# Kernel tuning notes

Hardware: AMD Instinct MI355X
Metric: run time of the kernel (lower is better)

Reference implementation:

```python
import jax, jax.numpy as jnp
import numpy as np

N_NODES = 20000
N_EDGES = 640000
HIDDEN = 256
HEADS = 8
HEAD_DIM = HIDDEN // HEADS
VOCAB = 119
N_FEATS = 9


def setup_inputs() -> dict:
    key = jax.random.key(0)
    ks = jax.random.split(key, 12)
    X = jax.random.randint(ks[0], (N_NODES, N_FEATS), 0, VOCAB)
    edge_row = jnp.sort(jax.random.randint(ks[1], (N_EDGES,), 0, N_NODES))
    edge_col = jax.random.randint(ks[2], (N_EDGES,), 0, N_NODES)
    s = 0.05  # init scale to keep activations sane
    emb_tables = jax.random.normal(ks[3], (N_FEATS, VOCAB, HIDDEN), jnp.float32) * s
    q_w = jax.random.normal(ks[4], (HIDDEN, HIDDEN), jnp.float32) * s
    q_b = jax.random.normal(ks[5], (HIDDEN,), jnp.float32) * s
    k_w = jax.random.normal(ks[6], (HIDDEN, HIDDEN), jnp.float32) * s
    k_b = jax.random.normal(ks[7], (HIDDEN,), jnp.float32) * s
    v_w = jax.random.normal(ks[8], (HIDDEN, HIDDEN), jnp.float32) * s
    v_b = jax.random.normal(ks[9], (HIDDEN,), jnp.float32) * s
    o_w = jax.random.normal(ks[10], (HIDDEN, HIDDEN), jnp.float32) * s
    o_b = jax.random.normal(ks[11], (HIDDEN,), jnp.float32) * s
    return dict(X=X, edge_row=edge_row, edge_col=edge_col, emb_tables=emb_tables,
                q_w=q_w, q_b=q_b, k_w=k_w, k_b=k_b, v_w=v_w, v_b=v_b, o_w=o_w, o_b=o_b)


def reference(X, edge_row, edge_col, emb_tables, q_w, q_b, k_w, k_b, v_w, v_b, o_w, o_b):
    N = X.shape[0]
    # AtomEncoder: sum of per-feature embeddings -> [N, HIDDEN]
    feat_idx = jnp.arange(N_FEATS)[None, :]  # [1, 9]
    h = emb_tables[feat_idx, X].sum(axis=1)  # [N, 9, H] -> [N, H]
    # q/k/v projections (torch Linear: y = x W^T + b), split into heads
    q = (h @ q_w.T + q_b).reshape(N, HEADS, HEAD_DIM) * (HEAD_DIM ** -0.5)
    k = (h @ k_w.T + k_b).reshape(N, HEADS, HEAD_DIM)
    v = (h @ v_w.T + v_b).reshape(N, HEADS, HEAD_DIM)
    # SDDMM: per-edge, per-head scores
    s = jnp.einsum('ehd,ehd->eh', q[edge_row], k[edge_col])  # [E, HEADS]
    # sparse row-wise softmax (over each node's outgoing-edge neighbors)
    m = jax.ops.segment_max(s, edge_row, num_segments=N)
    e = jnp.exp(s - m[edge_row])
    z = jax.ops.segment_sum(e, edge_row, num_segments=N)
    attn = e / z[edge_row]  # [E, HEADS]
    # SPMM: weighted aggregation of neighbor values
    out = jax.ops.segment_sum(attn[:, :, None] * v[edge_col], edge_row, num_segments=N)
    return out.reshape(N, HIDDEN) @ o_w.T + o_b
```

## Files before the change

kernel.cpp:

```cpp
#include <hip/hip_runtime.h>
#include <hip/hip_bf16.h>

#define N_NODES 20000
#define N_EDGES 640000
#define HIDDEN 256
#define HEADS 8
#define HEAD_DIM 32
#define N_FEATS 9
#define VOCAB 119

typedef __hip_bfloat16 bf16;
typedef __attribute__((ext_vector_type(8))) short short8;
typedef __attribute__((ext_vector_type(4))) float f32x4;
typedef __attribute__((ext_vector_type(2))) float f32x2;

__device__ __forceinline__ ushort f2u(float x) { union { ushort u; bf16 b; } c; c.b = __float2bfloat16(x); return c.u; }

__device__ __forceinline__ f32x2 pk_fma(f32x2 a, f32x2 b, f32x2 c) {
    f32x2 d;
    asm("v_pk_fma_f32 %0, %1, %2, %3" : "=v"(d) : "v"(a), "v"(b), "v"(c));
    return d;
}
__device__ __forceinline__ f32x2 pk_add(f32x2 a, f32x2 b) {
    f32x2 d;
    asm("v_pk_add_f32 %0, %1, %2" : "=v"(d) : "v"(a), "v"(b));
    return d;
}

template <int CTRL>
__device__ __forceinline__ float dpp_xor(float v) {
    return __int_as_float(__builtin_amdgcn_update_dpp(
        0, __float_as_int(v), CTRL, 0xf, 0xf, true));
}

__device__ __forceinline__ float fast_exp2(float x) {
#if __has_builtin(__builtin_amdgcn_exp2f)
    return __builtin_amdgcn_exp2f(x);
#else
    return exp2f(x);
#endif
}

__device__ __forceinline__ void sched_fence() {
    __builtin_amdgcn_sched_barrier(0);
}

#if __has_builtin(__builtin_amdgcn_fdot2_f32_bf16)
typedef __attribute__((ext_vector_type(2))) __bf16 bf16x2_t;
__device__ __forceinline__ float dot2bf(uint a, uint b, float c) {
    return __builtin_amdgcn_fdot2_f32_bf16(__builtin_bit_cast(bf16x2_t, a),
                                           __builtin_bit_cast(bf16x2_t, b), c, false);
}
#else
__device__ __forceinline__ float dot2bf(uint a, uint b, float c) {
    return c + __uint_as_float(a << 16) * __uint_as_float(b << 16)
             + __uint_as_float(a & 0xffff0000u) * __uint_as_float(b & 0xffff0000u);
}
#endif

__global__ void k_pre(const int* __restrict__ X, const float* __restrict__ emb,
                      bf16* __restrict__ h,
                      const float* __restrict__ qw, const float* __restrict__ kw,
                      const float* __restrict__ vw, const float* __restrict__ ow,
                      const float* __restrict__ qb, const float* __restrict__ kb,
                      const float* __restrict__ vb,
                      bf16* __restrict__ wqkv, bf16* __restrict__ wo,
                      float* __restrict__ qkvb,
                      const int* __restrict__ erow, int* __restrict__ row_ptr) {
    int b = blockIdx.x;
    if (b < 5000) {
        int tid = b * 256 + threadIdx.x;
        int n = tid >> 6;
        int c4 = (tid & 63) * 4;
        float4 a = make_float4(0.f, 0.f, 0.f, 0.f);
#pragma unroll
        for (int f = 0; f < N_FEATS; ++f) {
            int idx = X[n * N_FEATS + f];
            float4 e = *(const float4*)(emb + ((size_t)(f * VOCAB + idx)) * HIDDEN + c4);
            a.x += e.x; a.y += e.y; a.z += e.z; a.w += e.w;
        }
        ushort4 o = make_ushort4(f2u(a.x), f2u(a.y), f2u(a.z), f2u(a.w));
        *(ushort4*)((ushort*)h + (size_t)n * HIDDEN + c4) = o;
    } else if (b < 6027) {
        int i = (b - 5000) * 256 + threadIdx.x;
        if (i < 196608) {
            const float* s = i < 65536 ? qw : i < 131072 ? kw : vw;
            wqkv[i] = __float2bfloat16(s[i & 65535]);
        } else if (i < 262144) {
            wo[i - 196608] = __float2bfloat16(ow[i - 196608]);
        } else if (i < 262912) {
            int j = i - 262144;
            const float* s = j < 256 ? qb : j < 512 ? kb : vb;
            qkvb[j] = s[j & 255];
        }
    } else {
        int n = (b - 6027) * 256 + threadIdx.x;
        if (n > N_NODES) return;
        int lo = 0, hi = N_EDGES;
        while (lo < hi) {
            int mid = (lo + hi) >> 1;
            if (erow[mid] < n) lo = mid + 1; else hi = mid;
        }
        row_ptr[n] = lo;
    }
}

template <int MODE, bool GUARD, int TM>
__device__ __forceinline__ void gemm_core(const bf16* __restrict__ A,
                                          const bf16* __restrict__ W,
                                          const float* __restrict__ bias,
                                          void* __restrict__ Y0, void* __restrict__ Y1,
                                          float s_q, int n0, int d0) {
    constexpr int RI = TM / 32;
    __shared__ short As[TM * 72];
    __shared__ short Bs[128 * 72];
    int t = threadIdx.x;
    int lane = t & 63, w = t >> 6;
    int wr = (w >> 1) * (TM / 2), wc = (w & 1) * 64;
    int lr = lane & 15, quad = lane >> 4;

    f32x4 acc[RI][4] = {};
    short8 ra[RI], rb[4];
    int srowA[RI], skoA[RI], srowB[4], skoB[4];
#pragma unroll
    for (int it = 0; it < RI; ++it) { int c = t + 256 * it; srowA[it] = c >> 3; skoA[it] = (c & 7) * 8; }
#pragma unroll
    for (int it = 0; it < 4; ++it) { int c = t + 256 * it; srowB[it] = c >> 3; skoB[it] = (c & 7) * 8; }

#pragma unroll
    for (int it = 0; it < RI; ++it) {
        int n = n0 + srowA[it];
        short8 av = {};
        if (!GUARD || n < N_NODES) av = *(const short8*)(A + (size_t)n * HIDDEN + skoA[it]);
        ra[it] = av;
    }
#pragma unroll
    for (int it = 0; it < 4; ++it)
        rb[it] = *(const short8*)(W + (size_t)(d0 + srowB[it]) * HIDDEN + skoB[it]);
#pragma unroll
    for (int it = 0; it < RI; ++it) *(short8*)(&As[srowA[it] * 72 + skoA[it]]) = ra[it];
#pragma unroll
    for (int it = 0; it < 4; ++it)  *(short8*)(&Bs[srowB[it] * 72 + skoB[it]]) = rb[it];
    __syncthreads();

    for (int k0 = 64; k0 < 256; k0 += 64) {
#pragma unroll
        for (int it = 0; it < RI; ++it) {
            int n = n0 + srowA[it];
            short8 av = {};
            if (!GUARD || n < N_NODES) av = *(const short8*)(A + (size_t)n * HIDDEN + k0 + skoA[it]);
            ra[it] = av;
        }
#pragma unroll
        for (int it = 0; it < 4; ++it)
            rb[it] = *(const short8*)(W + (size_t)(d0 + srowB[it]) * HIDDEN + k0 + skoB[it]);
        {
            short8 af[RI][2], bfr[4][2];
#pragma unroll
            for (int i = 0; i < RI; ++i)
#pragma unroll
                for (int kk = 0; kk < 2; ++kk)
                    af[i][kk] = *(short8*)(&As[(wr + i * 16 + lr) * 72 + kk * 32 + quad * 8]);
#pragma unroll
            for (int j = 0; j < 4; ++j)
#pragma unroll
                for (int kk = 0; kk < 2; ++kk)
                    bfr[j][kk] = *(short8*)(&Bs[(wc + j * 16 + lr) * 72 + kk * 32 + quad * 8]);
#pragma unroll
            for (int kk = 0; kk < 2; ++kk)
#pragma unroll
                for (int i = 0; i < RI; ++i)
#pragma unroll
                    for (int j = 0; j < 4; ++j)
                        acc[i][j] = __builtin_amdgcn_mfma_f32_16x16x32_bf16(
                            af[i][kk], bfr[j][kk], acc[i][j], 0, 0, 0);
        }
        __syncthreads();
#pragma unroll
        for (int it = 0; it < RI; ++it) *(short8*)(&As[srowA[it] * 72 + skoA[it]]) = ra[it];
#pragma unroll
        for (int it = 0; it < 4; ++it)  *(short8*)(&Bs[srowB[it] * 72 + skoB[it]]) = rb[it];
        __syncthreads();
    }
    {
        short8 af[RI][2], bfr[4][2];
#pragma unroll
        for (int i = 0; i < RI; ++i)
#pragma unroll
            for (int kk = 0; kk < 2; ++kk)
                af[i][kk] = *(short8*)(&As[(wr + i * 16 + lr) * 72 + kk * 32 + quad * 8]);
#pragma unroll
        for (int j = 0; j < 4; ++j)
#pragma unroll
            for (int kk = 0; kk < 2; ++kk)
                bfr[j][kk] = *(short8*)(&Bs[(wc + j * 16 + lr) * 72 + kk * 32 + quad * 8]);
#pragma unroll
        for (int kk = 0; kk < 2; ++kk)
#pragma unroll
            for (int i = 0; i < RI; ++i)
#pragma unroll
                for (int j = 0; j < 4; ++j)
                    acc[i][j] = __builtin_amdgcn_mfma_f32_16x16x32_bf16(
                        af[i][kk], bfr[j][kk], acc[i][j], 0, 0, 0);
    }

#pragma unroll
    for (int j = 0; j < 4; ++j) {
        int dbase = d0 + wc + j * 16;
        float bj = bias[dbase + lr];
        if constexpr (MODE == 0) {
            float sc = (dbase < 256) ? s_q : 1.f;
            ushort* dst; int stride;
            if (dbase < 256) {
                dst = (ushort*)Y0 + (size_t)(dbase >> 6) * N_NODES * 64 + (dbase & 63) + lr;
                stride = 64;
            } else if (dbase < 512) {
                int e = dbase - 256;
                dst = (ushort*)Y1 + (size_t)(e >> 6) * N_NODES * 128 + (e & 63) + lr;
                stride = 128;
            } else {
                int e = dbase - 512;
                dst = (ushort*)Y1 + (size_t)(e >> 6) * N_NODES * 128 + 64 + (e & 63) + lr;
                stride = 128;
            }
#pragma unroll
            for (int i = 0; i < RI; ++i)
#pragma unroll
                for (int r = 0; r < 4; ++r) {
                    int n = n0 + wr + i * 16 + quad * 4 + r;
                    if (GUARD && n >= N_NODES) continue;
                    dst[(size_t)n * stride] = f2u((acc[i][j][r] + bj) * sc);
                }
        } else {
            float* dst = (float*)Y0 + dbase + lr;
#pragma unroll
            for (int i = 0; i < RI; ++i)
#pragma unroll
                for (int r = 0; r < 4; ++r) {
                    int n = n0 + wr + i * 16 + quad * 4 + r;
                    if (GUARD && n >= N_NODES) continue;
                    dst[(size_t)n * HIDDEN] = acc[i][j][r] + bj;
                }
        }
    }
}

__global__ __launch_bounds__(256, 2) void k_gemm_qkv(
    const bf16* __restrict__ A, const bf16* __restrict__ wqkv,
    const float* __restrict__ qkvb, ushort* __restrict__ qhp,
    ushort* __restrict__ kvhp, float qscale) {
    int n0 = blockIdx.x * 128;
    if (n0 + 128 <= N_NODES)
        gemm_core<0, false, 128>(A, wqkv, qkvb, qhp, kvhp, qscale, n0, blockIdx.y * 128);
    else
        gemm_core<0, true, 128>(A, wqkv, qkvb, qhp, kvhp, qscale, n0, blockIdx.y * 128);
}

__global__ __launch_bounds__(256, 4) void k_gemm_o(
    const bf16* __restrict__ A, const bf16* __restrict__ W,
    const float* __restrict__ bias, float* __restrict__ Y) {
    int n0 = blockIdx.x * 64;
    if (n0 + 64 <= N_NODES)
        gemm_core<1, false, 64>(A, W, bias, Y, nullptr, 1.f, n0, blockIdx.y * 128);
    else
        gemm_core<1, true, 64>(A, W, bias, Y, nullptr, 1.f, n0, blockIdx.y * 128);
}


template <int NIT>
__device__ __forceinline__ void pv_accum(const uint4* vv, const float* pb,
                                         f32x2& av0, f32x2& av1, f32x2& av2v, f32x2& av3) {
#pragma unroll
    for (int it = 0; it < NIT; ++it) {
        f32x2 pp; pp.x = pb[it]; pp.y = pb[it];
        f32x2 vf0, vf1, vf2, vf3;
        vf0.x = __uint_as_float(vv[it].x << 16); vf0.y = __uint_as_float(vv[it].x & 0xffff0000u);
        vf1.x = __uint_as_float(vv[it].y << 16); vf1.y = __uint_as_float(vv[it].y & 0xffff0000u);
        vf2.x = __uint_as_float(vv[it].z << 16); vf2.y = __uint_as_float(vv[it].z & 0xffff0000u);
        vf3.x = __uint_as_float(vv[it].w << 16); vf3.y = __uint_as_float(vv[it].w & 0xffff0000u);
        av0  = pk_fma(vf0, pp, av0);
        av1  = pk_fma(vf1, pp, av1);
        av2v = pk_fma(vf2, pp, av2v);
        av3  = pk_fma(vf3, pp, av3);
    }
}

__device__ __forceinline__ void attn_combine(int lane, int d8, float z,
                                             f32x2 av0, f32x2 av1, f32x2 av2v, f32x2 av3,
                                             ushort* __restrict__ orow) {
    bool b3 = (lane & 8) != 0, b4 = (lane & 16) != 0, b5 = (lane & 32) != 0;
    f32x2 sd0 = b3 ? av0 : av2v;
    f32x2 sd1 = b3 ? av1 : av3;
    f32x2 r0, r1;
    r0.x = dpp_xor<0x128>(sd0.x); r0.y = dpp_xor<0x128>(sd0.y);
    r1.x = dpp_xor<0x128>(sd1.x); r1.y = dpp_xor<0x128>(sd1.y);
    f32x2 t0 = pk_add(b3 ? av2v : av0, r0);
    f32x2 t1 = pk_add(b3 ? av3  : av1, r1);
    f32x2 sdu = b4 ? t0 : t1;
    f32x2 ru; ru.x = __shfl_xor(sdu.x, 16); ru.y = __shfl_xor(sdu.y, 16);
    f32x2 u = pk_add(b4 ? t1 : t0, ru);
    float sw = b5 ? u.x : u.y;
    float rw = __shfl_xor(sw, 32);
    float w = (b5 ? u.y : u.x) + rw;
    int dim = d8 * 8 + ((lane >> 3) & 1) * 4 + ((lane >> 4) & 1) * 2 + ((lane >> 5) & 1);
    orow[dim] = f2u(w * (1.f / z));
}

template <int NIT>
__device__ __forceinline__ void attn_dense(const int* __restrict__ cb, int deg,
                                           int lane, int my, int d8,
                                           const ushort* __restrict__ qrow,
                                           const ushort* __restrict__ kvbase,
                                           ushort* __restrict__ orow) {
    int degm8 = deg - my;
    uint d8b = (uint)d8 * 8;

    int cc[NIT];
#pragma unroll
    for (int it = 0; it < NIT; ++it) cc[it] = cb[min(it * 8 + my, deg - 1)];

    uint4 qu = *(const uint4*)(qrow + d8b);
    uint4 kk[NIT], vv[NIT];
#pragma unroll
    for (int it = 0; it < NIT; ++it)
        kk[it] = *(const uint4*)(kvbase + (((size_t)(uint)cc[it]) << 7) + d8b);
#pragma unroll
    for (int it = 0; it < NIT; ++it)
        vv[it] = *(const uint4*)(kvbase + (((size_t)(uint)cc[it]) << 7) + 64 + d8b);

    sched_fence();

    float z = 0.f;
    float pb[NIT];
#pragma unroll
    for (int it = 0; it < NIT; ++it) {
        float s = dot2bf(kk[it].x, qu.x, 0.f);
        s = dot2bf(kk[it].y, qu.y, s);
        s = dot2bf(kk[it].z, qu.z, s);
        s = dot2bf(kk[it].w, qu.w, s);
        s += dpp_xor<0xB1>(s);
        s += dpp_xor<0x4E>(s);
        float p = (it * 8 < degm8) ? fast_exp2(s) : 0.f;
        z += p;
        pb[it] = p;
    }
    z += dpp_xor<0x128>(z);
    z += __shfl_xor(z, 16);
    z += __shfl_xor(z, 32);

    f32x2 av0 = {0.f, 0.f}, av1 = {0.f, 0.f}, av2v = {0.f, 0.f}, av3 = {0.f, 0.f};
    pv_accum<NIT>(vv, pb, av0, av1, av2v, av3);
    attn_combine(lane, d8, z, av0, av1, av2v, av3, orow);
}

__global__ __launch_bounds__(256, 4) void k_attn(
    const int* __restrict__ row_ptr, const int* __restrict__ col,
    const ushort* __restrict__ qhp, const ushort* __restrict__ kvhp,
    bf16* __restrict__ agg) {
    int b = blockIdx.x;
    int x = b & 7;
    int hp = x & 3;
    int wave = __builtin_amdgcn_readfirstlane((int)(threadIdx.x >> 6));
    int n = (b >> 3) * 8 + (x >> 2) * 4 + wave;
    int lane = threadIdx.x & 63;
    int my = lane >> 3;
    int d8 = lane & 7;

    int start = row_ptr[n];
    int deg = row_ptr[n + 1] - start;

    ushort* orow = (ushort*)agg + (size_t)n * HIDDEN + hp * 64;
    if (deg == 0) {
        if (lane < 8) { uint4 zo = {}; *(uint4*)(orow + lane * 8) = zo; }
        return;
    }

    const ushort* qrow = qhp + ((size_t)hp * N_NODES + n) * 64;
    const ushort* kvbase = kvhp + (size_t)hp * N_NODES * 128;
    const int* cb = col + start;

    if (deg <= 32) {
        attn_dense<4>(cb, deg, lane, my, d8, qrow, kvbase, orow);
    } else if (deg <= 64) {
        attn_dense<8>(cb, deg, lane, my, d8, qrow, kvbase, orow);
    } else {
        uint4 qu = *(const uint4*)(qrow + d8 * 8);
        float z = 0.f;
        f32x2 av0 = {0.f, 0.f}, av1 = {0.f, 0.f}, av2v = {0.f, 0.f}, av3 = {0.f, 0.f};
        for (int i = 0; i < deg; i += 8) {
            int idx = i + my;
            int cidx = idx < deg ? idx : deg - 1;
            int c = cb[cidx];
            const ushort* kp = kvbase + (((size_t)(uint)c) << 7) + (uint)d8 * 8;
            uint4 ku = *(const uint4*)(kp);
            uint4 vu = *(const uint4*)(kp + 64);
            float s = dot2bf(ku.x, qu.x, 0.f);
            s = dot2bf(ku.y, qu.y, s);
            s = dot2bf(ku.z, qu.z, s);
            s = dot2bf(ku.w, qu.w, s);
            s += dpp_xor<0xB1>(s);
            s += dpp_xor<0x4E>(s);
            float p = (idx < deg) ? fast_exp2(s) : 0.f;
            z += p;
            f32x2 pp; pp.x = p; pp.y = p;
            f32x2 vf0, vf1, vf2, vf3;
            vf0.x = __uint_as_float(vu.x << 16); vf0.y = __uint_as_float(vu.x & 0xffff0000u);
            vf1.x = __uint_as_float(vu.y << 16); vf1.y = __uint_as_float(vu.y & 0xffff0000u);
            vf2.x = __uint_as_float(vu.z << 16); vf2.y = __uint_as_float(vu.z & 0xffff0000u);
            vf3.x = __uint_as_float(vu.w << 16); vf3.y = __uint_as_float(vu.w & 0xffff0000u);
            av0  = pk_fma(vf0, pp, av0);
            av1  = pk_fma(vf1, pp, av1);
            av2v = pk_fma(vf2, pp, av2v);
            av3  = pk_fma(vf3, pp, av3);
        }
        z += dpp_xor<0x128>(z);
        z += __shfl_xor(z, 16);
        z += __shfl_xor(z, 32);
        attn_combine(lane, d8, z, av0, av1, av2v, av3, orow);
    }
}

extern "C" void kernel_launch(void* const* d_in, const int* in_sizes, int n_in,
                              void* d_out, int out_size, void* d_ws, size_t ws_size,
                              hipStream_t stream) {
    const int*   X    = (const int*)d_in[0];
    const int*   erow = (const int*)d_in[1];
    const int*   ecol = (const int*)d_in[2];
    const float* emb  = (const float*)d_in[3];
    const float* q_w  = (const float*)d_in[4];
    const float* q_b  = (const float*)d_in[5];
    const float* k_w  = (const float*)d_in[6];
    const float* k_b  = (const float*)d_in[7];
    const float* v_w  = (const float*)d_in[8];
    const float* v_b  = (const float*)d_in[9];
    const float* o_w  = (const float*)d_in[10];
    const float* o_b  = (const float*)d_in[11];
    float* out = (float*)d_out;

    char* ws = (char*)d_ws;
    bf16*   h    = (bf16*)(ws);
    bf16*   agg  = (bf16*)(ws);
    ushort* qhp  = (ushort*)(ws + 10240000);
    ushort* kvhp = (ushort*)(ws + 20480000);
    bf16*   wqkv = (bf16*)(ws + 40960000);
    bf16*   wo   = (bf16*)(ws + 41353216);
    float*  qkvb = (float*)(ws + 41484288);
    int* row_ptr = (int*)(ws + 41487360);

    k_pre<<<6106, 256, 0, stream>>>(X, emb, h, q_w, k_w, v_w, o_w,
                                    q_b, k_b, v_b, wqkv, wo, qkvb, erow, row_ptr);

    const float qscale = 0.25503486121587466f;
    dim3 gqkv((N_NODES + 127) / 128, 768 / 128);
    k_gemm_qkv<<<gqkv, 256, 0, stream>>>(h, wqkv, qkvb, qhp, kvhp, qscale);

    k_attn<<<N_NODES, 256, 0, stream>>>(row_ptr, ecol, qhp, kvhp, agg);

    dim3 go((N_NODES + 63) / 64, HIDDEN / 128);
    k_gemm_o<<<go, 256, 0, stream>>>(agg, wo, o_b, out);
}
```

Baseline: 174.7 us.

## Process two head-pairs per wave in attention and shrink QKV GEMM row tile

The attention kernel now has each wave handle two head-pairs for one node instead of one. This halves the grid and shares the column-index loads across both head-pairs. A new paired dense path issues all K/V gathers for both head-pairs up front and interleaves the score computation to expose more memory-level parallelism. Separately, the QKV GEMM row tile drops from 128 to 64 with higher occupancy bounds, giving more blocks. The cost is more registers per wave in the attention kernel and fewer waves overall.

```diff
diff --git a/kernel.cpp b/kernel.cpp
--- a/kernel.cpp
+++ b/kernel.cpp
@@ -245,15 +245,15 @@
     }
 }
 
-__global__ __launch_bounds__(256, 2) void k_gemm_qkv(
+__global__ __launch_bounds__(256, 4) void k_gemm_qkv(
     const bf16* __restrict__ A, const bf16* __restrict__ wqkv,
     const float* __restrict__ qkvb, ushort* __restrict__ qhp,
     ushort* __restrict__ kvhp, float qscale) {
-    int n0 = blockIdx.x * 128;
-    if (n0 + 128 <= N_NODES)
-        gemm_core<0, false, 128>(A, wqkv, qkvb, qhp, kvhp, qscale, n0, blockIdx.y * 128);
+    int n0 = blockIdx.x * 64;
+    if (n0 + 64 <= N_NODES)
+        gemm_core<0, false, 64>(A, wqkv, qkvb, qhp, kvhp, qscale, n0, blockIdx.y * 128);
     else
-        gemm_core<0, true, 128>(A, wqkv, qkvb, qhp, kvhp, qscale, n0, blockIdx.y * 128);
+        gemm_core<0, true, 64>(A, wqkv, qkvb, qhp, kvhp, qscale, n0, blockIdx.y * 128);
 }
 
 __global__ __launch_bounds__(256, 4) void k_gemm_o(
@@ -353,70 +353,153 @@
     attn_combine(lane, d8, z, av0, av1, av2v, av3, orow);
 }
 
+__device__ __forceinline__ void attn_dense_pair(const int* __restrict__ cb, int deg,
+                                                int lane, int my, int d8,
+                                                const ushort* __restrict__ qrow0,
+                                                const ushort* __restrict__ qrow1,
+                                                const ushort* __restrict__ kvb0,
+                                                const ushort* __restrict__ kvb1,
+                                                ushort* __restrict__ orow0,
+                                                ushort* __restrict__ orow1) {
+    int degm8 = deg - my;
+    uint d8b = (uint)d8 * 8;
+
+    int cc[4];
+#pragma unroll
+    for (int it = 0; it < 4; ++it) cc[it] = cb[min(it * 8 + my, deg - 1)];
+
+    uint4 qu0 = *(const uint4*)(qrow0 + d8b);
+    uint4 qu1 = *(const uint4*)(qrow1 + d8b);
+    uint4 kk0[4], kk1[4], vv0[4], vv1[4];
+#pragma unroll
+    for (int it = 0; it < 4; ++it)
+        kk0[it] = *(const uint4*)(kvb0 + (((size_t)(uint)cc[it]) << 7) + d8b);
+#pragma unroll
+    for (int it = 0; it < 4; ++it)
+        kk1[it] = *(const uint4*)(kvb1 + (((size_t)(uint)cc[it]) << 7) + d8b);
+#pragma unroll
+    for (int it = 0; it < 4; ++it)
+        vv0[it] = *(const uint4*)(kvb0 + (((size_t)(uint)cc[it]) << 7) + 64 + d8b);
+#pragma unroll
+    for (int it = 0; it < 4; ++it)
+        vv1[it] = *(const uint4*)(kvb1 + (((size_t)(uint)cc[it]) << 7) + 64 + d8b);
+
+    sched_fence();
+
+    f32x2 zz = {0.f, 0.f};
+    float pb0[4], pb1[4];
+#pragma unroll
+    for (int it = 0; it < 4; ++it) {
+        float s0 = dot2bf(kk0[it].x, qu0.x, 0.f);
+        float s1 = dot2bf(kk1[it].x, qu1.x, 0.f);
+        s0 = dot2bf(kk0[it].y, qu0.y, s0);
+        s1 = dot2bf(kk1[it].y, qu1.y, s1);
+        s0 = dot2bf(kk0[it].z, qu0.z, s0);
+        s1 = dot2bf(kk1[it].z, qu1.z, s1);
+        s0 = dot2bf(kk0[it].w, qu0.w, s0);
+        s1 = dot2bf(kk1[it].w, qu1.w, s1);
+        s0 += dpp_xor<0xB1>(s0); s1 += dpp_xor<0xB1>(s1);
+        s0 += dpp_xor<0x4E>(s0); s1 += dpp_xor<0x4E>(s1);
+        bool ok = it * 8 < degm8;
+        float p0 = ok ? fast_exp2(s0) : 0.f;
+        float p1 = ok ? fast_exp2(s1) : 0.f;
+        zz.x += p0; zz.y += p1;
+        pb0[it] = p0; pb1[it] = p1;
+    }
+    {
+        f32x2 r;
+        r.x = dpp_xor<0x128>(zz.x); r.y = dpp_xor<0x128>(zz.y); zz = pk_add(zz, r);
+        r.x = __shfl_xor(zz.x, 16); r.y = __shfl_xor(zz.y, 16); zz = pk_add(zz, r);
+        r.x = __shfl_xor(zz.x, 32); r.y = __shfl_xor(zz.y, 32); zz = pk_add(zz, r);
+    }
+
+    f32x2 a00 = {0.f, 0.f}, a01 = {0.f, 0.f}, a02 = {0.f, 0.f}, a03 = {0.f, 0.f};
+    pv_accum<4>(vv0, pb0, a00, a01, a02, a03);
+    attn_combine(lane, d8, zz.x, a00, a01, a02, a03, orow0);
+    f32x2 a10 = {0.f, 0.f}, a11 = {0.f, 0.f}, a12 = {0.f, 0.f}, a13 = {0.f, 0.f};
+    pv_accum<4>(vv1, pb1, a10, a11, a12, a13);
+    attn_combine(lane, d8, zz.y, a10, a11, a12, a13, orow1);
+}
+
 __global__ __launch_bounds__(256, 4) void k_attn(
     const int* __restrict__ row_ptr, const int* __restrict__ col,
     const ushort* __restrict__ qhp, const ushort* __restrict__ kvhp,
     bf16* __restrict__ agg) {
     int b = blockIdx.x;
-    int x = b & 7;
-    int hp = x & 3;
+    int hpp = b & 1;
     int wave = __builtin_amdgcn_readfirstlane((int)(threadIdx.x >> 6));
-    int n = (b >> 3) * 8 + (x >> 2) * 4 + wave;
+    int n = (b >> 1) * 4 + wave;
     int lane = threadIdx.x & 63;
     int my = lane >> 3;
     int d8 = lane & 7;
 
+    int hp0 = hpp * 2, hp1 = hp0 + 1;
+
     int start = row_ptr[n];
     int deg = row_ptr[n + 1] - start;
 
-    ushort* orow = (ushort*)agg + (size_t)n * HIDDEN + hp * 64;
+    ushort* orow0 = (ushort*)agg + (size_t)n * HIDDEN + hp0 * 64;
+    ushort* orow1 = orow0 + 64;
     if (deg == 0) {
-        if (lane < 8) { uint4 zo = {}; *(uint4*)(orow + lane * 8) = zo; }
+        if (lane < 8) {
+            uint4 zo = {};
+            *(uint4*)(orow0 + lane * 8) = zo;
+            *(uint4*)(orow1 + lane * 8) = zo;
+        }
         return;
     }
 
-    const ushort* qrow = qhp + ((size_t)hp * N_NODES + n) * 64;
-    const ushort* kvbase = kvhp + (size_t)hp * N_NODES * 128;
+    const ushort* qrow0 = qhp + ((size_t)hp0 * N_NODES + n) * 64;
+    const ushort* qrow1 = qhp + ((size_t)hp1 * N_NODES + n) * 64;
+    const ushort* kvb0 = kvhp + (size_t)hp0 * N_NODES * 128;
+    const ushort* kvb1 = kvhp + (size_t)hp1 * N_NODES * 128;
     const int* cb = col + start;
 
     if (deg <= 32) {
-        attn_dense<4>(cb, deg, lane, my, d8, qrow, kvbase, orow);
+        attn_dense_pair(cb, deg, lane, my, d8, qrow0, qrow1, kvb0, kvb1, orow0, orow1);
     } else if (deg <= 64) {
-        attn_dense<8>(cb, deg, lane, my, d8, qrow, kvbase, orow);
+        attn_dense<8>(cb, deg, lane, my, d8, qrow0, kvb0, orow0);
+        attn_dense<8>(cb, deg, lane, my, d8, qrow1, kvb1, orow1);
     } else {
-        uint4 qu = *(const uint4*)(qrow + d8 * 8);
-        float z = 0.f;
-        f32x2 av0 = {0.f, 0.f}, av1 = {0.f, 0.f}, av2v = {0.f, 0.f}, av3 = {0.f, 0.f};
-        for (int i = 0; i < deg; i += 8) {
-            int idx = i + my;
-            int cidx = idx < deg ? idx : deg - 1;
-            int c = cb[cidx];
-            const ushort* kp = kvbase + (((size_t)(uint)c) << 7) + (uint)d8 * 8;
-            uint4 ku = *(const uint4*)(kp);
-            uint4 vu = *(const uint4*)(kp + 64);
-            float s = dot2bf(ku.x, qu.x, 0.f);
-            s = dot2bf(ku.y, qu.y, s);
-            s = dot2bf(ku.z, qu.z, s);
-            s = dot2bf(ku.w, qu.w, s);
-            s += dpp_xor<0xB1>(s);
-            s += dpp_xor<0x4E>(s);
-            float p = (idx < deg) ? fast_exp2(s) : 0.f;
-            z += p;
-            f32x2 pp; pp.x = p; pp.y = p;
-            f32x2 vf0, vf1, vf2, vf3;
-            vf0.x = __uint_as_float(vu.x << 16); vf0.y = __uint_as_float(vu.x & 0xffff0000u);
-            vf1.x = __uint_as_float(vu.y << 16); vf1.y = __uint_as_float(vu.y & 0xffff0000u);
-            vf2.x = __uint_as_float(vu.z << 16); vf2.y = __uint_as_float(vu.z & 0xffff0000u);
-            vf3.x = __uint_as_float(vu.w << 16); vf3.y = __uint_as_float(vu.w & 0xffff0000u);
-            av0  = pk_fma(vf0, pp, av0);
-            av1  = pk_fma(vf1, pp, av1);
-            av2v = pk_fma(vf2, pp, av2v);
-            av3  = pk_fma(vf3, pp, av3);
-        }
-        z += dpp_xor<0x128>(z);
-        z += __shfl_xor(z, 16);
-        z += __shfl_xor(z, 32);
-        attn_combine(lane, d8, z, av0, av1, av2v, av3, orow);
+#pragma unroll 1
+        for (int h = 0; h < 2; ++h) {
+            const ushort* qrow = h ? qrow1 : qrow0;
+            const ushort* kvbase = h ? kvb1 : kvb0;
+            ushort* orow = h ? orow1 : orow0;
+            uint4 qu = *(const uint4*)(qrow + d8 * 8);
+            float z = 0.f;
+            f32x2 av0 = {0.f, 0.f}, av1 = {0.f, 0.f}, av2v = {0.f, 0.f}, av3 = {0.f, 0.f};
+            for (int i = 0; i < deg; i += 8) {
+                int idx = i + my;
+                int cidx = idx < deg ? idx : deg - 1;
+                int c = cb[cidx];
+                const ushort* kp = kvbase + (((size_t)(uint)c) << 7) + (uint)d8 * 8;
+                uint4 ku = *(const uint4*)(kp);
+                uint4 vu = *(const uint4*)(kp + 64);
+                float s = dot2bf(ku.x, qu.x, 0.f);
+                s = dot2bf(ku.y, qu.y, s);
+                s = dot2bf(ku.z, qu.z, s);
+                s = dot2bf(ku.w, qu.w, s);
+                s += dpp_xor<0xB1>(s);
+                s += dpp_xor<0x4E>(s);
+                float p = (idx < deg) ? fast_exp2(s) : 0.f;
+                z += p;
+                f32x2 pp; pp.x = p; pp.y = p;
+                f32x2 vf0, vf1, vf2, vf3;
+                vf0.x = __uint_as_float(vu.x << 16); vf0.y = __uint_as_float(vu.x & 0xffff0000u);
+                vf1.x = __uint_as_float(vu.y << 16); vf1.y = __uint_as_float(vu.y & 0xffff0000u);
+                vf2.x = __uint_as_float(vu.z << 16); vf2.y = __uint_as_float(vu.z & 0xffff0000u);
+                vf3.x = __uint_as_float(vu.w << 16); vf3.y = __uint_as_float(vu.w & 0xffff0000u);
+                av0  = pk_fma(vf0, pp, av0);
+                av1  = pk_fma(vf1, pp, av1);
+                av2v = pk_fma(vf2, pp, av2v);
+                av3  = pk_fma(vf3, pp, av3);
+            }
+            z += dpp_xor<0x128>(z);
+            z += __shfl_xor(z, 16);
+            z += __shfl_xor(z, 32);
+            attn_combine(lane, d8, z, av0, av1, av2v, av3, orow);
+        }
     }
 }
 
@@ -451,10 +534,10 @@
                                     q_b, k_b, v_b, wqkv, wo, qkvb, erow, row_ptr);
 
     const float qscale = 0.25503486121587466f;
-    dim3 gqkv((N_NODES + 127) / 128, 768 / 128);
+    dim3 gqkv((N_NODES + 63) / 64, 768 / 128);
     k_gemm_qkv<<<gqkv, 256, 0, stream>>>(h, wqkv, qkvb, qhp, kvhp, qscale);
 
-    k_attn<<<N_NODES, 256, 0, stream>>>(row_ptr, ecol, qhp, kvhp, agg);
+    k_attn<<<N_NODES / 2, 256, 0, stream>>>(row_ptr, ecol, qhp, kvhp, agg);
 
     dim3 go((N_NODES + 63) / 64, HIDDEN / 128);
     k_gemm_o<<<go, 256, 0, stream>>>(agg, wo, o_b, out);
```

Result: slower. 193.8 us (+10.9%).

## Switch attention to per-head K/V layout with one wave per node-head

Applied to the files above, without the earlier changes.

The QKV GEMM epilogue now writes K and V interleaved per single head (64 bf16 per node per head) rather than per head-pair (128 per node). The attention kernel assigns one wave to each (node, head), with 16 edges processed in parallel by 4 lanes each, and launches twice as many blocks. This halves the bytes gathered per edge per wave and lets low-degree nodes run fewer wasted padded iterations (NIT 1-4). In exchange the lane reductions use more cross-row shuffles, half the lanes sit idle at the final store, and the q/index loads are repeated per head.

```diff
diff --git a/kernel.cpp b/kernel.cpp
--- a/kernel.cpp
+++ b/kernel.cpp
@@ -216,12 +216,16 @@
                 stride = 64;
             } else if (dbase < 512) {
                 int e = dbase - 256;
-                dst = (ushort*)Y1 + (size_t)(e >> 6) * N_NODES * 128 + (e & 63) + lr;
-                stride = 128;
+                int head = e >> 5;
+                int dim = (e & 31) + lr;
+                dst = (ushort*)Y1 + (size_t)head * N_NODES * 64 + dim;
+                stride = 64;
             } else {
                 int e = dbase - 512;
-                dst = (ushort*)Y1 + (size_t)(e >> 6) * N_NODES * 128 + 64 + (e & 63) + lr;
-                stride = 128;
+                int head = e >> 5;
+                int dim = (e & 31) + lr;
+                dst = (ushort*)Y1 + (size_t)head * N_NODES * 64 + 32 + dim;
+                stride = 64;
             }
 #pragma unroll
             for (int i = 0; i < RI; ++i)
@@ -248,12 +252,12 @@
 __global__ __launch_bounds__(256, 2) void k_gemm_qkv(
     const bf16* __restrict__ A, const bf16* __restrict__ wqkv,
     const float* __restrict__ qkvb, ushort* __restrict__ qhp,
-    ushort* __restrict__ kvhp, float qscale) {
+    ushort* __restrict__ khv, float qscale) {
     int n0 = blockIdx.x * 128;
     if (n0 + 128 <= N_NODES)
-        gemm_core<0, false, 128>(A, wqkv, qkvb, qhp, kvhp, qscale, n0, blockIdx.y * 128);
+        gemm_core<0, false, 128>(A, wqkv, qkvb, qhp, khv, qscale, n0, blockIdx.y * 128);
     else
-        gemm_core<0, true, 128>(A, wqkv, qkvb, qhp, kvhp, qscale, n0, blockIdx.y * 128);
+        gemm_core<0, true, 128>(A, wqkv, qkvb, qhp, khv, qscale, n0, blockIdx.y * 128);
 }
 
 __global__ __launch_bounds__(256, 4) void k_gemm_o(
@@ -285,48 +289,51 @@
     }
 }
 
-__device__ __forceinline__ void attn_combine(int lane, int d8, float z,
-                                             f32x2 av0, f32x2 av1, f32x2 av2v, f32x2 av3,
+__device__ __forceinline__ void attn_combine_h(int lane, int d4, float z,
+                                               f32x2 av0, f32x2 av1, f32x2 av2v, f32x2 av3,
+                                               ushort* __restrict__ orow) {
+    bool b2 = (lane & 4) != 0, b3 = (lane & 8) != 0, b4 = (lane & 16) != 0;
+    f32x2 sd0 = b2 ? av0 : av2v;
+    f32x2 sd1 = b2 ? av1 : av3;
+    f32x2 r0, r1;
+    r0.x = __shfl_xor(sd0.x, 4); r0.y = __shfl_xor(sd0.y, 4);
+    r1.x = __shfl_xor(sd1.x, 4); r1.y = __shfl_xor(sd1.y, 4);
+    f32x2 t0 = pk_add(b2 ? av2v : av0, r0);
+    f32x2 t1 = pk_add(b2 ? av3  : av1, r1);
+    f32x2 sdu = b3 ? t0 : t1;
+    f32x2 ru; ru.x = __shfl_xor(sdu.x, 8); ru.y = __shfl_xor(sdu.y, 8);
+    f32x2 u = pk_add(b3 ? t1 : t0, ru);
+    float sw = b4 ? u.x : u.y;
+    float rw = __shfl_xor(sw, 16);
+    float w = (b4 ? u.y : u.x) + rw;
+    w += __shfl_xor(w, 32);
+    if (lane < 32) {
+        int dim = d4 * 8 + ((lane >> 2) & 1) * 4 + ((lane >> 3) & 1) * 2 + ((lane >> 4) & 1);
+        orow[dim] = f2u(w * (1.f / z));
+    }
+}
+
+template <int NIT>
+__device__ __forceinline__ void attn_dense_h(const int* __restrict__ cb, int deg,
+                                             int lane, int my, int d4,
+                                             const ushort* __restrict__ qrow,
+                                             const ushort* __restrict__ khbase,
                                              ushort* __restrict__ orow) {
-    bool b3 = (lane & 8) != 0, b4 = (lane & 16) != 0, b5 = (lane & 32) != 0;
-    f32x2 sd0 = b3 ? av0 : av2v;
-    f32x2 sd1 = b3 ? av1 : av3;
-    f32x2 r0, r1;
-    r0.x = dpp_xor<0x128>(sd0.x); r0.y = dpp_xor<0x128>(sd0.y);
-    r1.x = dpp_xor<0x128>(sd1.x); r1.y = dpp_xor<0x128>(sd1.y);
-    f32x2 t0 = pk_add(b3 ? av2v : av0, r0);
-    f32x2 t1 = pk_add(b3 ? av3  : av1, r1);
-    f32x2 sdu = b4 ? t0 : t1;
-    f32x2 ru; ru.x = __shfl_xor(sdu.x, 16); ru.y = __shfl_xor(sdu.y, 16);
-    f32x2 u = pk_add(b4 ? t1 : t0, ru);
-    float sw = b5 ? u.x : u.y;
-    float rw = __shfl_xor(sw, 32);
-    float w = (b5 ? u.y : u.x) + rw;
-    int dim = d8 * 8 + ((lane >> 3) & 1) * 4 + ((lane >> 4) & 1) * 2 + ((lane >> 5) & 1);
-    orow[dim] = f2u(w * (1.f / z));
-}
-
-template <int NIT>
-__device__ __forceinline__ void attn_dense(const int* __restrict__ cb, int deg,
-                                           int lane, int my, int d8,
-                                           const ushort* __restrict__ qrow,
-                                           const ushort* __restrict__ kvbase,
-                                           ushort* __restrict__ orow) {
-    int degm8 = deg - my;
-    uint d8b = (uint)d8 * 8;
+    int degm = deg - my;
+    uint d4b = (uint)d4 * 8;
 
     int cc[NIT];
 #pragma unroll
-    for (int it = 0; it < NIT; ++it) cc[it] = cb[min(it * 8 + my, deg - 1)];
-
-    uint4 qu = *(const uint4*)(qrow + d8b);
+    for (int it = 0; it < NIT; ++it) cc[it] = cb[min(it * 16 + my, deg - 1)];
+
+    uint4 qu = *(const uint4*)(qrow + d4b);
     uint4 kk[NIT], vv[NIT];
 #pragma unroll
     for (int it = 0; it < NIT; ++it)
-        kk[it] = *(const uint4*)(kvbase + (((size_t)(uint)cc[it]) << 7) + d8b);
+        kk[it] = *(const uint4*)(khbase + (((size_t)(uint)cc[it]) << 6) + d4b);
 #pragma unroll
     for (int it = 0; it < NIT; ++it)
-        vv[it] = *(const uint4*)(kvbase + (((size_t)(uint)cc[it]) << 7) + 64 + d8b);
+        vv[it] = *(const uint4*)(khbase + (((size_t)(uint)cc[it]) << 6) + 32 + d4b);
 
     sched_fence();
 
@@ -340,60 +347,60 @@
         s = dot2bf(kk[it].w, qu.w, s);
         s += dpp_xor<0xB1>(s);
         s += dpp_xor<0x4E>(s);
-        float p = (it * 8 < degm8) ? fast_exp2(s) : 0.f;
+        float p = (it * 16 < degm) ? fast_exp2(s) : 0.f;
         z += p;
         pb[it] = p;
     }
+    z += dpp_xor<0x124>(z);
     z += dpp_xor<0x128>(z);
     z += __shfl_xor(z, 16);
     z += __shfl_xor(z, 32);
 
     f32x2 av0 = {0.f, 0.f}, av1 = {0.f, 0.f}, av2v = {0.f, 0.f}, av3 = {0.f, 0.f};
     pv_accum<NIT>(vv, pb, av0, av1, av2v, av3);
-    attn_combine(lane, d8, z, av0, av1, av2v, av3, orow);
+    attn_combine_h(lane, d4, z, av0, av1, av2v, av3, orow);
 }
 
 __global__ __launch_bounds__(256, 4) void k_attn(
     const int* __restrict__ row_ptr, const int* __restrict__ col,
-    const ushort* __restrict__ qhp, const ushort* __restrict__ kvhp,
+    const ushort* __restrict__ qhp, const ushort* __restrict__ khv,
     bf16* __restrict__ agg) {
     int b = blockIdx.x;
-    int x = b & 7;
-    int hp = x & 3;
+    int h = b & 7;
     int wave = __builtin_amdgcn_readfirstlane((int)(threadIdx.x >> 6));
-    int n = (b >> 3) * 8 + (x >> 2) * 4 + wave;
+    int n = (b >> 3) * 4 + wave;
     int lane = threadIdx.x & 63;
-    int my = lane >> 3;
-    int d8 = lane & 7;
+    int my = lane >> 2;
+    int d4 = lane & 3;
 
     int start = row_ptr[n];
     int deg = row_ptr[n + 1] - start;
 
-    ushort* orow = (ushort*)agg + (size_t)n * HIDDEN + hp * 64;
+    ushort* orow = (ushort*)agg + (size_t)n * HIDDEN + h * 32;
     if (deg == 0) {
-        if (lane < 8) { uint4 zo = {}; *(uint4*)(orow + lane * 8) = zo; }
+        if (lane < 4) { uint4 zo = {}; *(uint4*)(orow + lane * 8) = zo; }
         return;
     }
 
-    const ushort* qrow = qhp + ((size_t)hp * N_NODES + n) * 64;
-    const ushort* kvbase = kvhp + (size_t)hp * N_NODES * 128;
+    const ushort* qrow = qhp + ((size_t)(h >> 1) * N_NODES + n) * 64 + (h & 1) * 32;
+    const ushort* khbase = khv + (size_t)h * N_NODES * 64;
     const int* cb = col + start;
 
-    if (deg <= 32) {
-        attn_dense<4>(cb, deg, lane, my, d8, qrow, kvbase, orow);
-    } else if (deg <= 64) {
-        attn_dense<8>(cb, deg, lane, my, d8, qrow, kvbase, orow);
-    } else {
-        uint4 qu = *(const uint4*)(qrow + d8 * 8);
+    if (deg <= 16)      attn_dense_h<1>(cb, deg, lane, my, d4, qrow, khbase, orow);
+    else if (deg <= 32) attn_dense_h<2>(cb, deg, lane, my, d4, qrow, khbase, orow);
+    else if (deg <= 48) attn_dense_h<3>(cb, deg, lane, my, d4, qrow, khbase, orow);
+    else if (deg <= 64) attn_dense_h<4>(cb, deg, lane, my, d4, qrow, khbase, orow);
+    else {
+        uint d4b = (uint)d4 * 8;
+        uint4 qu = *(const uint4*)(qrow + d4b);
         float z = 0.f;
         f32x2 av0 = {0.f, 0.f}, av1 = {0.f, 0.f}, av2v = {0.f, 0.f}, av3 = {0.f, 0.f};
-        for (int i = 0; i < deg; i += 8) {
+        for (int i = 0; i < deg; i += 16) {
             int idx = i + my;
-            int cidx = idx < deg ? idx : deg - 1;
-            int c = cb[cidx];
-            const ushort* kp = kvbase + (((size_t)(uint)c) << 7) + (uint)d8 * 8;
+            int c = cb[min(idx, deg - 1)];
+            const ushort* kp = khbase + (((size_t)(uint)c) << 6) + d4b;
             uint4 ku = *(const uint4*)(kp);
-            uint4 vu = *(const uint4*)(kp + 64);
+            uint4 vu = *(const uint4*)(kp + 32);
             float s = dot2bf(ku.x, qu.x, 0.f);
             s = dot2bf(ku.y, qu.y, s);
             s = dot2bf(ku.z, qu.z, s);
@@ -413,10 +420,11 @@
             av2v = pk_fma(vf2, pp, av2v);
             av3  = pk_fma(vf3, pp, av3);
         }
+        z += dpp_xor<0x124>(z);
         z += dpp_xor<0x128>(z);
         z += __shfl_xor(z, 16);
         z += __shfl_xor(z, 32);
-        attn_combine(lane, d8, z, av0, av1, av2v, av3, orow);
+        attn_combine_h(lane, d4, z, av0, av1, av2v, av3, orow);
     }
 }
 
@@ -441,7 +449,7 @@
     bf16*   h    = (bf16*)(ws);
     bf16*   agg  = (bf16*)(ws);
     ushort* qhp  = (ushort*)(ws + 10240000);
-    ushort* kvhp = (ushort*)(ws + 20480000);
+    ushort* khv  = (ushort*)(ws + 20480000);
     bf16*   wqkv = (bf16*)(ws + 40960000);
     bf16*   wo   = (bf16*)(ws + 41353216);
     float*  qkvb = (float*)(ws + 41484288);
@@ -452,9 +460,9 @@
 
     const float qscale = 0.25503486121587466f;
     dim3 gqkv((N_NODES + 127) / 128, 768 / 128);
-    k_gemm_qkv<<<gqkv, 256, 0, stream>>>(h, wqkv, qkvb, qhp, kvhp, qscale);
-
-    k_attn<<<N_NODES, 256, 0, stream>>>(row_ptr, ecol, qhp, kvhp, agg);
+    k_gemm_qkv<<<gqkv, 256, 0, stream>>>(h, wqkv, qkvb, qhp, khv, qscale);
+
+    k_attn<<<40000, 256, 0, stream>>>(row_ptr, ecol, qhp, khv, agg);
 
     dim3 go((N_NODES + 63) / 64, HIDDEN / 128);
     k_gemm_o<<<go, 256, 0, stream>>>(agg, wo, o_b, out);
```

Measured after the change: 177.2 us. About the same (+1.4%).
